# Kernel tuning notes

Hardware: AMD Instinct MI355X
Metric: run time of the kernel (lower is better)

The kernel has to match this reference:

```python
import jax, jax.numpy as jnp
import numpy as np

N = 64            # SSM state size
L = 4194304       # l_max = sequence length (2**22)
M = 4096          # chunk length for kernel construction
NCHUNK = L // M   # 1024 chunks


def setup_inputs() -> dict:
    key = jax.random.key(0)
    k0, k1, k2, k3, k4 = jax.random.split(key, 5)
    u = jax.random.normal(k0, (L, 1), jnp.float32)
    # lecun_normal: std = 1/sqrt(fan_in)
    W = jax.random.normal(k1, (N, N), jnp.float32) * np.float32(1.0 / np.sqrt(N))
    # spectral shift so bilinear-discretized Ab is stable over L steps
    A = W - 1.5 * jnp.eye(N, dtype=jnp.float32)
    B = jax.random.normal(k2, (N, 1), jnp.float32)  # fan_in = 1 -> std 1
    C = jax.random.normal(k3, (1, N), jnp.float32) * np.float32(1.0 / np.sqrt(N))
    D = jnp.ones((1,), jnp.float32)
    lo, hi = np.float32(np.log(1e-3)), np.float32(np.log(1e-1))
    log_step = jax.random.uniform(k4, (1,), jnp.float32, lo, hi)
    return {"u": u, "A": A, "B": B, "C": C, "D": D, "log_step": log_step}


def _ssm_forward(u, A, B, C, D, log_step):
    step = jnp.exp(log_step)[0]
    I = jnp.eye(N, dtype=A.dtype)
    # bilinear (Tustin) discretization
    BL = jnp.linalg.inv(I - A * (step / 2.0))
    Ab = BL @ (I + A * (step / 2.0))          # [N, N]
    Bb = (BL * step) @ B                      # [N, 1]
    Cb = C                                    # [1, N]

    # K[k] = Cb @ Ab^k @ Bb, k = 0..L-1, built in chunks of M:
    # X0[:, k] = Ab^k @ Bb for k < M
    def step_x(x, _):
        return Ab @ x, x
    _, xs = jax.lax.scan(step_x, Bb[:, 0], None, length=M)   # [M, N]
    X0 = xs.T                                                # [N, M]

    AbM = jnp.linalg.matrix_power(Ab, M)                     # Ab^M
    def step_p(P, _):
        return AbM @ P, Cb[0] @ P                            # row: Cb @ Ab^(j*M)
    _, cps = jax.lax.scan(step_p, I, None, length=NCHUNK)    # [NCHUNK, N]
    K = (cps @ X0).reshape(L, 1)                             # [L, 1]

    # FFT causal convolution (pad to 2L, pointwise multiply, crop)
    fft_size = 2 * L
    u_d = jnp.fft.rfft(jnp.pad(u, ((0, L), (0, 0))), n=fft_size, axis=0)
    K_d = jnp.fft.rfft(jnp.pad(K, ((0, L), (0, 0))), n=fft_size, axis=0)
    y = jnp.fft.irfft(u_d * K_d, n=fft_size, axis=0)[:L]
    return y + D * u


def reference(u, A, B, C, D, log_step):
    return _ssm_forward(u, A, B, C, D, log_step)
```

## Files before the change

kernel.cpp:

```cpp
#include <hip/hip_runtime.h>
#include <cmath>


#define NST 64
#define LSEQ 4194304
#define MC 256
#define NCHUNK (LSEQ / MC)
#define SEG 128
#define NSEG (NCHUNK / SEG)
#define NPOW 16

#define POW_OFF 0
#define BB_OFF (NPOW * 4096)
#define XCOL_OFF (BB_OFF + 64)
#define KL_OFF (XCOL_OFF + MC * 64)
#define RT_OFF (KL_OFF + MC)
#define F_OFF (RT_OFF + 64 * MC)
#define CARRY_OFF (F_OFF + NCHUNK * 64)
#define SEGINIT_OFF (CARRY_OFF + NSEG * 64)
#define WS_FLOATS (SEGINIT_OFF + NSEG * 64)

__device__ __forceinline__ float bcast(float x, int k) {
  return __int_as_float(__builtin_amdgcn_readlane(__float_as_int(x), k));
}

__global__ __launch_bounds__(1024) void k_setup(
    const float* __restrict__ A, const float* __restrict__ Bv,
    const float* __restrict__ Cv, const float* __restrict__ lstep,
    float* __restrict__ ws) {
  __shared__ __align__(16) float sm[8704];
  const int t = threadIdx.x;
  const float h = 0.5f * expf(lstep[0]);

  for (int idx = t; idx < 64 * 128; idx += 1024) {
    int r = idx >> 7, c = idx & 127;
    float v;
    if (c < 64)
      v = (r == c ? 1.0f : 0.0f) - h * A[r * 64 + c];
    else
      v = (r == (c - 64)) ? 1.0f : 0.0f;
    sm[r * 129 + c] = v;
  }
  __syncthreads();
  for (int k = 0; k < 64; ++k) {
    if (t < 64) sm[8256 + t] = sm[t * 129 + k];
    __syncthreads();
    float pinv = 1.0f / sm[8256 + k];
    if (t < 128) sm[k * 129 + t] *= pinv;
    __syncthreads();
    for (int idx = t; idx < 64 * 128; idx += 1024) {
      int r = idx >> 7, c = idx & 127;
      if (r != k) sm[r * 129 + c] -= sm[8256 + r] * sm[k * 129 + c];
    }
    __syncthreads();
  }

  for (int idx = t; idx < 4096; idx += 1024) {
    int r = idx >> 6, c = idx & 63;
    float acc = 0.f;
    for (int k = 0; k < 64; ++k) acc += sm[r * 129 + 64 + k] * A[k * 64 + c];
    ws[POW_OFF + r * 64 + c] = sm[r * 129 + 64 + c] + h * acc;
  }
  if (t < 64) {
    float acc = 0.f;
    for (int k = 0; k < 64; ++k) acc += sm[t * 129 + 64 + k] * Bv[k];
    ws[BB_OFF + t] = 2.0f * h * acc;
  }
  __syncthreads();

  for (int idx = t; idx < 4096; idx += 1024)
    sm[(idx >> 6) * 68 + (idx & 63)] = ws[POW_OFF + idx];
  __syncthreads();
  for (int s = 1; s < NPOW; ++s) {
    float* src = sm + ((s & 1) ? 0 : 4352);
    float* dst = sm + ((s & 1) ? 4352 : 0);
    const int r = t >> 4, c0 = (t & 15) << 2;
    float4 acc = {0.f, 0.f, 0.f, 0.f};
#pragma unroll 8
    for (int k = 0; k < 64; ++k) {
      float a = src[r * 68 + k];
      const float4 b = *(const float4*)&src[k * 68 + c0];
      acc.x += a * b.x; acc.y += a * b.y; acc.z += a * b.z; acc.w += a * b.w;
    }
    *(float4*)&dst[r * 68 + c0] = acc;
    *(float4*)&ws[POW_OFF + s * 4096 + r * 64 + c0] = acc;
    __syncthreads();
  }

  if (t < 64) {
    ws[XCOL_OFF + t] = ws[BB_OFF + t];
  } else if (t < 128) {
    int n = t - 64;
    float acc = 0.f;
    for (int k = 0; k < 64; ++k) acc += Cv[k] * ws[POW_OFF + k * 64 + n];
    ws[RT_OFF + n * MC + 0] = acc;
  }
  for (int s = 0; s < 8; ++s) {
    __syncthreads();
    for (int idx = t; idx < 4096; idx += 1024)
      sm[(idx >> 6) * 65 + (idx & 63)] = ws[POW_OFF + s * 4096 + idx];
    __syncthreads();
    const int cnt = 1 << s;
    for (int idx = t; idx < cnt * 64; idx += 1024) {
      int ir = cnt + (idx >> 6), n = idx & 63, isrc = ir - cnt;
      float xv = 0.f, rv = 0.f;
#pragma unroll 8
      for (int k = 0; k < 64; ++k) {
        xv += sm[n * 65 + k] * ws[XCOL_OFF + isrc * 64 + k];
        rv += sm[k * 65 + n] * ws[RT_OFF + k * MC + isrc];
      }
      ws[XCOL_OFF + ir * 64 + n] = xv;
      ws[RT_OFF + n * MC + ir] = rv;
    }
  }
  __syncthreads();

  {
    const int w = t >> 6, lane = t & 63;
    for (int i = w; i < MC; i += 16) {
      float p = Cv[lane] * ws[XCOL_OFF + i * 64 + lane];
#pragma unroll
      for (int m = 32; m >= 1; m >>= 1) p += __shfl_xor(p, m, 64);
      if (lane == 0) ws[KL_OFF + i] = p;
    }
  }
}

__global__ __launch_bounds__(256) void k_f(const float* __restrict__ u,
                                           float* __restrict__ ws) {
  __shared__ __align__(16) float us[16 * MC];
  const int t = threadIdx.x;
  const int c0 = blockIdx.x * 16;
  for (int idx = t; idx < 16 * MC; idx += 256)
    us[idx] = u[(size_t)c0 * MC + idx];
  __syncthreads();
  const int n = t & 63, g = t >> 6;
  const float* xc = ws + XCOL_OFF;
  const float* ug = us + g * 4 * MC;
  float a0 = 0.f, a1 = 0.f, a2 = 0.f, a3 = 0.f;
  for (int j = 0; j < MC; j += 4) {
    float x0 = xc[(MC - 1 - j) * 64 + n];
    float x1 = xc[(MC - 2 - j) * 64 + n];
    float x2 = xc[(MC - 3 - j) * 64 + n];
    float x3 = xc[(MC - 4 - j) * 64 + n];
    {
      const float4 uv = *(const float4*)&ug[0 * MC + j];
      a0 += x0 * uv.x + x1 * uv.y + x2 * uv.z + x3 * uv.w;
    }
    {
      const float4 uv = *(const float4*)&ug[1 * MC + j];
      a1 += x0 * uv.x + x1 * uv.y + x2 * uv.z + x3 * uv.w;
    }
    {
      const float4 uv = *(const float4*)&ug[2 * MC + j];
      a2 += x0 * uv.x + x1 * uv.y + x2 * uv.z + x3 * uv.w;
    }
    {
      const float4 uv = *(const float4*)&ug[3 * MC + j];
      a3 += x0 * uv.x + x1 * uv.y + x2 * uv.z + x3 * uv.w;
    }
  }
  float* Fb = ws + F_OFF + (size_t)(c0 + g * 4) * 64;
  Fb[0 * 64 + n] = a0;
  Fb[1 * 64 + n] = a1;
  Fb[2 * 64 + n] = a2;
  Fb[3 * 64 + n] = a3;
}

#define MATVEC_STEP(preg, xv, a0, a1, a2, a3)          \
  _Pragma("unroll") for (int k = 0; k < 64; k += 4) {  \
    a0 = fmaf(preg[k + 0], bcast(xv, k + 0), a0);      \
    a1 = fmaf(preg[k + 1], bcast(xv, k + 1), a1);      \
    a2 = fmaf(preg[k + 2], bcast(xv, k + 2), a2);      \
    a3 = fmaf(preg[k + 3], bcast(xv, k + 3), a3);      \
  }

__global__ __launch_bounds__(64) void k_scan1(float* __restrict__ ws) {
  __shared__ float Pl[64 * 65];
  const int n = threadIdx.x;
  for (int idx = n; idx < 4096; idx += 64)
    Pl[(idx >> 6) * 65 + (idx & 63)] = ws[POW_OFF + 8 * 4096 + idx];
  __syncthreads();
  float p[64];
#pragma unroll
  for (int k = 0; k < 64; ++k) p[k] = Pl[n * 65 + k];
  float x = 0.f;
  const float* Fp = ws + F_OFF + (size_t)blockIdx.x * SEG * 64;
  float fv = Fp[n];
  for (int c = 0; c < SEG; ++c) {
    float fnext = Fp[(c < SEG - 1 ? c + 1 : c) * 64 + n];
    float a0 = 0.f, a1 = 0.f, a2 = 0.f, a3 = 0.f;
    MATVEC_STEP(p, x, a0, a1, a2, a3)
    x = ((a0 + a1) + (a2 + a3)) + fv;
    fv = fnext;
  }
  ws[CARRY_OFF + blockIdx.x * 64 + n] = x;
}

__global__ __launch_bounds__(64) void k_scantop(float* __restrict__ ws) {
  __shared__ float Ql[64 * 65];
  const int n = threadIdx.x;
  for (int idx = n; idx < 4096; idx += 64)
    Ql[(idx >> 6) * 65 + (idx & 63)] = ws[POW_OFF + 15 * 4096 + idx];
  __syncthreads();
  float q[64];
#pragma unroll
  for (int k = 0; k < 64; ++k) q[k] = Ql[n * 65 + k];
  float x = 0.f;
  float cv = ws[CARRY_OFF + n];
  for (int s = 0; s < NSEG; ++s) {
    float cnext = ws[CARRY_OFF + (s < NSEG - 1 ? s + 1 : s) * 64 + n];
    ws[SEGINIT_OFF + s * 64 + n] = x;
    float a0 = 0.f, a1 = 0.f, a2 = 0.f, a3 = 0.f;
    MATVEC_STEP(q, x, a0, a1, a2, a3)
    x = ((a0 + a1) + (a2 + a3)) + cv;
    cv = cnext;
  }
}

__global__ __launch_bounds__(64) void k_scan2(float* __restrict__ ws) {
  __shared__ float Pl[64 * 65];
  const int n = threadIdx.x;
  for (int idx = n; idx < 4096; idx += 64)
    Pl[(idx >> 6) * 65 + (idx & 63)] = ws[POW_OFF + 8 * 4096 + idx];
  __syncthreads();
  float p[64];
#pragma unroll
  for (int k = 0; k < 64; ++k) p[k] = Pl[n * 65 + k];
  float x = ws[SEGINIT_OFF + blockIdx.x * 64 + n];
  float* Fp = ws + F_OFF + (size_t)blockIdx.x * SEG * 64;
  float fv = Fp[n];
  for (int c = 0; c < SEG; ++c) {
    float fnext = Fp[(c < SEG - 1 ? c + 1 : c) * 64 + n];
    Fp[c * 64 + n] = x;
    float a0 = 0.f, a1 = 0.f, a2 = 0.f, a3 = 0.f;
    MATVEC_STEP(p, x, a0, a1, a2, a3)
    x = ((a0 + a1) + (a2 + a3)) + fv;
    fv = fnext;
  }
}

__global__ __launch_bounds__(256) void k_final(const float* __restrict__ u,
                                               const float* __restrict__ Dv,
                                               const float* __restrict__ ws,
                                               float* __restrict__ out) {
  __shared__ __align__(16) float us[8 * MC];
  __shared__ __align__(16) float kl[MC];
  __shared__ __align__(16) float xin[8 * 64];
  const int t = threadIdx.x;
  const int c0 = blockIdx.x * 8;
  for (int idx = t; idx < 8 * MC; idx += 256)
    us[idx] = u[(size_t)c0 * MC + idx];
  kl[t] = ws[KL_OFF + t];
  for (int idx = t; idx < 8 * 64; idx += 256)
    xin[idx] = ws[F_OFF + (size_t)c0 * 64 + idx];
  __syncthreads();

  float acc[8];
#pragma unroll
  for (int cc = 0; cc < 8; ++cc) acc[cc] = 0.f;

  const float* rt = ws + RT_OFF;
#pragma unroll 4
  for (int nn = 0; nn < 64; nn += 4) {
    float r0 = rt[(nn + 0) * MC + t];
    float r1 = rt[(nn + 1) * MC + t];
    float r2 = rt[(nn + 2) * MC + t];
    float r3 = rt[(nn + 3) * MC + t];
#pragma unroll
    for (int cc = 0; cc < 8; ++cc) {
      const float4 xv = *(const float4*)&xin[cc * 64 + nn];
      acc[cc] += r0 * xv.x + r1 * xv.y + r2 * xv.z + r3 * xv.w;
    }
  }

  const int i = t;
  int j = 0;
  for (; j + 3 <= i; j += 4) {
    float k0 = kl[i - j], k1 = kl[i - j - 1], k2 = kl[i - j - 2],
          k3 = kl[i - j - 3];
#pragma unroll
    for (int cc = 0; cc < 8; ++cc) {
      const float4 uv = *(const float4*)&us[cc * MC + j];
      acc[cc] += k0 * uv.x + k1 * uv.y + k2 * uv.z + k3 * uv.w;
    }
  }
  for (; j <= i; ++j) {
    float kv = kl[i - j];
#pragma unroll
    for (int cc = 0; cc < 8; ++cc) acc[cc] += kv * us[cc * MC + j];
  }

  const float D0 = Dv[0];
#pragma unroll
  for (int cc = 0; cc < 8; ++cc)
    out[(size_t)(c0 + cc) * MC + i] = acc[cc] + D0 * us[cc * MC + i];
}

extern "C" void kernel_launch(void* const* d_in, const int* in_sizes, int n_in,
                              void* d_out, int out_size, void* d_ws,
                              size_t ws_size, hipStream_t stream) {
  (void)in_sizes; (void)n_in; (void)out_size; (void)ws_size;
  const float* u = (const float*)d_in[0];
  const float* A = (const float*)d_in[1];
  const float* B = (const float*)d_in[2];
  const float* C = (const float*)d_in[3];
  const float* D = (const float*)d_in[4];
  const float* ls = (const float*)d_in[5];
  float* ws = (float*)d_ws;
  float* out = (float*)d_out;

  hipLaunchKernelGGL(k_setup, dim3(1), dim3(1024), 0, stream, A, B, C, ls, ws);
  hipLaunchKernelGGL(k_f, dim3(NCHUNK / 16), dim3(256), 0, stream, u, ws);
  hipLaunchKernelGGL(k_scan1, dim3(NSEG), dim3(64), 0, stream, ws);
  hipLaunchKernelGGL(k_scantop, dim3(1), dim3(64), 0, stream, ws);
  hipLaunchKernelGGL(k_scan2, dim3(NSEG), dim3(64), 0, stream, ws);
  hipLaunchKernelGGL(k_final, dim3(NCHUNK / 8), dim3(256), 0, stream, u, D, ws,
                     out);
}
```

Before: 444.1 us.

## Restructure setup kernel: fused Gauss-Jordan solve, register-tiled powers, parallel Krylov generation

Rewrites the single-block setup kernel. Gauss-Jordan now reduces [I-hA | I+hA | 2hB] together, so Ab and Bb fall out directly without separate matmuls, and the elimination updates use float4 over only the remaining columns. Matrix squaring uses an 8x4 register tile over row and transposed copies, and stores only the powers that are needed (4, 8, 15). The X and R Krylov columns are built by 16 waves in parallel from seeds spaced Ab^16 apart, using register-resident matvecs, instead of log-doubling through global memory. It trims a serial, latency-bound setup phase at the cost of more shared memory and more code complexity.

```diff
diff --git a/kernel.cpp b/kernel.cpp
--- a/kernel.cpp
+++ b/kernel.cpp
@@ -8,14 +8,19 @@
 #define NCHUNK (LSEQ / MC)
 #define SEG 128
 #define NSEG (NCHUNK / SEG)
-#define NPOW 16
-
-#define POW_OFF 0
-#define BB_OFF (NPOW * 4096)
-#define XCOL_OFF (BB_OFF + 64)
-#define KL_OFF (XCOL_OFF + MC * 64)
-#define RT_OFF (KL_OFF + MC)
-#define F_OFF (RT_OFF + 64 * MC)
+
+#define ABR_OFF 0
+#define ABT_OFF 4096
+#define P4R_OFF 8192
+#define P4T_OFF 12288
+#define P8_OFF 16384
+#define P15_OFF 20480
+#define BB_OFF 24576
+#define KL_OFF 24640
+#define XCOL_OFF 24896
+#define RTT_OFF 41280
+#define RT_OFF 57664
+#define F_OFF 74048
 #define CARRY_OFF (F_OFF + NCHUNK * 64)
 #define SEGINIT_OFF (CARRY_OFF + NSEG * 64)
 #define WS_FLOATS (SEGINIT_OFF + NSEG * 64)
@@ -23,102 +28,227 @@
 __device__ __forceinline__ float bcast(float x, int k) {
   return __int_as_float(__builtin_amdgcn_readlane(__float_as_int(x), k));
 }
+
+__device__ __forceinline__ float matvec64(const float4 (&m)[16], float x) {
+  float a0 = 0.f, a1 = 0.f, a2 = 0.f, a3 = 0.f;
+#pragma unroll
+  for (int kq = 0; kq < 16; ++kq) {
+    a0 = fmaf(m[kq].x, bcast(x, 4 * kq + 0), a0);
+    a1 = fmaf(m[kq].y, bcast(x, 4 * kq + 1), a1);
+    a2 = fmaf(m[kq].z, bcast(x, 4 * kq + 2), a2);
+    a3 = fmaf(m[kq].w, bcast(x, 4 * kq + 3), a3);
+  }
+  return ((a0 + a1) + (a2 + a3));
+}
+
+__device__ __forceinline__ void load_rows(float4 (&m)[16], const float* src,
+                                          int lane) {
+#pragma unroll
+  for (int kq = 0; kq < 16; ++kq)
+    m[kq] = *(const float4*)(src + (size_t)lane * 64 + kq * 4);
+}
+
+#define CGET(v, cj) ((cj) == 0 ? (v).x : (cj) == 1 ? (v).y : (cj) == 2 ? (v).z : (v).w)
 
 __global__ __launch_bounds__(1024) void k_setup(
     const float* __restrict__ A, const float* __restrict__ Bv,
     const float* __restrict__ Cv, const float* __restrict__ lstep,
     float* __restrict__ ws) {
-  __shared__ __align__(16) float sm[8704];
+  __shared__ __align__(16) float sm[14592];
+  float* colbuf = sm + 12352;
+  float* xs = sm + 12416;
+  float* rs = sm + 13504;
   const int t = threadIdx.x;
+  const int w = t >> 6, lane = t & 63;
   const float h = 0.5f * expf(lstep[0]);
 
-  for (int idx = t; idx < 64 * 128; idx += 1024) {
-    int r = idx >> 7, c = idx & 127;
-    float v;
-    if (c < 64)
-      v = (r == c ? 1.0f : 0.0f) - h * A[r * 64 + c];
-    else
-      v = (r == (c - 64)) ? 1.0f : 0.0f;
-    sm[r * 129 + c] = v;
-  }
-  __syncthreads();
-  for (int k = 0; k < 64; ++k) {
-    if (t < 64) sm[8256 + t] = sm[t * 129 + k];
-    __syncthreads();
-    float pinv = 1.0f / sm[8256 + k];
-    if (t < 128) sm[k * 129 + t] *= pinv;
-    __syncthreads();
-    for (int idx = t; idx < 64 * 128; idx += 1024) {
-      int r = idx >> 7, c = idx & 127;
-      if (r != k) sm[r * 129 + c] -= sm[8256 + r] * sm[k * 129 + c];
-    }
-    __syncthreads();
-  }
-
+  {
+    const int r = t >> 4;
+    for (int c = t & 15; c < 144; c += 16) {
+      float v = 0.f;
+      if (c < 64)
+        v = (r == c ? 1.0f : 0.0f) - h * A[r * 64 + c];
+      else if (c < 128)
+        v = (r == (c - 64) ? 1.0f : 0.0f) + h * A[r * 64 + (c - 64)];
+      else if (c == 128)
+        v = 2.0f * h * Bv[r];
+      sm[r * 144 + c] = v;
+    }
+  }
+  __syncthreads();
+  {
+    float4* G4 = (float4*)sm;
+    for (int k = 0; k < 64; ++k) {
+      if (t < 64) colbuf[t] = sm[t * 144 + k];
+      __syncthreads();
+      const float pinv = 1.0f / colbuf[k];
+      const int r = lane;
+      const float mr = colbuf[r] * pinv;
+      for (int q = (k >> 2) + w; q <= 32; q += 16) {
+        float4 pr = G4[k * 36 + q];
+        float4 g = G4[r * 36 + q];
+        if (r == k) {
+          g.x = pr.x * pinv; g.y = pr.y * pinv;
+          g.z = pr.z * pinv; g.w = pr.w * pinv;
+        } else {
+          g.x = fmaf(-mr, pr.x, g.x); g.y = fmaf(-mr, pr.y, g.y);
+          g.z = fmaf(-mr, pr.z, g.z); g.w = fmaf(-mr, pr.w, g.w);
+        }
+        G4[r * 36 + q] = g;
+      }
+      __syncthreads();
+    }
+  }
   for (int idx = t; idx < 4096; idx += 1024) {
     int r = idx >> 6, c = idx & 63;
-    float acc = 0.f;
-    for (int k = 0; k < 64; ++k) acc += sm[r * 129 + 64 + k] * A[k * 64 + c];
-    ws[POW_OFF + r * 64 + c] = sm[r * 129 + 64 + c] + h * acc;
-  }
-  if (t < 64) {
-    float acc = 0.f;
-    for (int k = 0; k < 64; ++k) acc += sm[t * 129 + 64 + k] * Bv[k];
-    ws[BB_OFF + t] = 2.0f * h * acc;
-  }
-  __syncthreads();
-
-  for (int idx = t; idx < 4096; idx += 1024)
-    sm[(idx >> 6) * 68 + (idx & 63)] = ws[POW_OFF + idx];
-  __syncthreads();
-  for (int s = 1; s < NPOW; ++s) {
-    float* src = sm + ((s & 1) ? 0 : 4352);
-    float* dst = sm + ((s & 1) ? 4352 : 0);
-    const int r = t >> 4, c0 = (t & 15) << 2;
-    float4 acc = {0.f, 0.f, 0.f, 0.f};
+    ws[ABR_OFF + idx] = sm[r * 144 + 64 + c];
+  }
+  if (t < 64) ws[BB_OFF + t] = sm[t * 144 + 128];
+  __syncthreads();
+
+  {
+    float* AR = sm;
+    float* AT = sm + 4096;
+    float* tr = sm + 8192;
+    for (int idx = t; idx < 4096; idx += 1024) {
+      float v = ws[ABR_OFF + idx];
+      AR[idx] = v;
+      tr[(idx & 63) * 65 + (idx >> 6)] = v;
+    }
+    __syncthreads();
+    for (int idx = t; idx < 4096; idx += 1024) {
+      float v = tr[(idx >> 6) * 65 + (idx & 63)];
+      AT[idx] = v;
+      ws[ABT_OFF + idx] = v;
+    }
+  }
+  __syncthreads();
+
+  {
+    float4* AR4 = (float4*)sm;
+    float4* AT4 = (float4*)(sm + 4096);
+    const bool active = t < 128;
+    const int r0 = (t >> 4) << 3;
+    const int c0q = t & 15;
+    for (int s = 1; s <= 15; ++s) {
+      float4 acc[8];
+#pragma unroll
+      for (int j = 0; j < 8; ++j) acc[j] = {0.f, 0.f, 0.f, 0.f};
+      if (active) {
 #pragma unroll 8
-    for (int k = 0; k < 64; ++k) {
-      float a = src[r * 68 + k];
-      const float4 b = *(const float4*)&src[k * 68 + c0];
-      acc.x += a * b.x; acc.y += a * b.y; acc.z += a * b.z; acc.w += a * b.w;
-    }
-    *(float4*)&dst[r * 68 + c0] = acc;
-    *(float4*)&ws[POW_OFF + s * 4096 + r * 64 + c0] = acc;
-    __syncthreads();
-  }
-
-  if (t < 64) {
-    ws[XCOL_OFF + t] = ws[BB_OFF + t];
-  } else if (t < 128) {
-    int n = t - 64;
-    float acc = 0.f;
-    for (int k = 0; k < 64; ++k) acc += Cv[k] * ws[POW_OFF + k * 64 + n];
-    ws[RT_OFF + n * MC + 0] = acc;
-  }
-  for (int s = 0; s < 8; ++s) {
-    __syncthreads();
-    for (int idx = t; idx < 4096; idx += 1024)
-      sm[(idx >> 6) * 65 + (idx & 63)] = ws[POW_OFF + s * 4096 + idx];
-    __syncthreads();
-    const int cnt = 1 << s;
-    for (int idx = t; idx < cnt * 64; idx += 1024) {
-      int ir = cnt + (idx >> 6), n = idx & 63, isrc = ir - cnt;
-      float xv = 0.f, rv = 0.f;
-#pragma unroll 8
-      for (int k = 0; k < 64; ++k) {
-        xv += sm[n * 65 + k] * ws[XCOL_OFF + isrc * 64 + k];
-        rv += sm[k * 65 + n] * ws[RT_OFF + k * MC + isrc];
+        for (int k = 0; k < 64; ++k) {
+          const float4 b = AR4[k * 16 + c0q];
+          const float4 a0 = AT4[k * 16 + (r0 >> 2)];
+          const float4 a1 = AT4[k * 16 + (r0 >> 2) + 1];
+          acc[0].x = fmaf(a0.x, b.x, acc[0].x); acc[0].y = fmaf(a0.x, b.y, acc[0].y);
+          acc[0].z = fmaf(a0.x, b.z, acc[0].z); acc[0].w = fmaf(a0.x, b.w, acc[0].w);
+          acc[1].x = fmaf(a0.y, b.x, acc[1].x); acc[1].y = fmaf(a0.y, b.y, acc[1].y);
+          acc[1].z = fmaf(a0.y, b.z, acc[1].z); acc[1].w = fmaf(a0.y, b.w, acc[1].w);
+          acc[2].x = fmaf(a0.z, b.x, acc[2].x); acc[2].y = fmaf(a0.z, b.y, acc[2].y);
+          acc[2].z = fmaf(a0.z, b.z, acc[2].z); acc[2].w = fmaf(a0.z, b.w, acc[2].w);
+          acc[3].x = fmaf(a0.w, b.x, acc[3].x); acc[3].y = fmaf(a0.w, b.y, acc[3].y);
+          acc[3].z = fmaf(a0.w, b.z, acc[3].z); acc[3].w = fmaf(a0.w, b.w, acc[3].w);
+          acc[4].x = fmaf(a1.x, b.x, acc[4].x); acc[4].y = fmaf(a1.x, b.y, acc[4].y);
+          acc[4].z = fmaf(a1.x, b.z, acc[4].z); acc[4].w = fmaf(a1.x, b.w, acc[4].w);
+          acc[5].x = fmaf(a1.y, b.x, acc[5].x); acc[5].y = fmaf(a1.y, b.y, acc[5].y);
+          acc[5].z = fmaf(a1.y, b.z, acc[5].z); acc[5].w = fmaf(a1.y, b.w, acc[5].w);
+          acc[6].x = fmaf(a1.z, b.x, acc[6].x); acc[6].y = fmaf(a1.z, b.y, acc[6].y);
+          acc[6].z = fmaf(a1.z, b.z, acc[6].z); acc[6].w = fmaf(a1.z, b.w, acc[6].w);
+          acc[7].x = fmaf(a1.w, b.x, acc[7].x); acc[7].y = fmaf(a1.w, b.y, acc[7].y);
+          acc[7].z = fmaf(a1.w, b.z, acc[7].z); acc[7].w = fmaf(a1.w, b.w, acc[7].w);
+        }
       }
-      ws[XCOL_OFF + ir * 64 + n] = xv;
-      ws[RT_OFF + n * MC + ir] = rv;
-    }
-  }
-  __syncthreads();
-
-  {
-    const int w = t >> 6, lane = t & 63;
+      __syncthreads();
+      if (active) {
+#pragma unroll
+        for (int j = 0; j < 8; ++j) AR4[(r0 + j) * 16 + c0q] = acc[j];
+#pragma unroll
+        for (int cj = 0; cj < 4; ++cj) {
+          float4 lo = {CGET(acc[0], cj), CGET(acc[1], cj), CGET(acc[2], cj),
+                       CGET(acc[3], cj)};
+          float4 hi = {CGET(acc[4], cj), CGET(acc[5], cj), CGET(acc[6], cj),
+                       CGET(acc[7], cj)};
+          AT4[(c0q * 4 + cj) * 16 + (r0 >> 2)] = lo;
+          AT4[(c0q * 4 + cj) * 16 + (r0 >> 2) + 1] = hi;
+          if (s == 4) {
+            *(float4*)&ws[P4T_OFF + (c0q * 4 + cj) * 64 + r0] = lo;
+            *(float4*)&ws[P4T_OFF + (c0q * 4 + cj) * 64 + r0 + 4] = hi;
+          }
+        }
+        if (s == 4 || s == 8 || s == 15) {
+          const int off = (s == 4) ? P4R_OFF : (s == 8) ? P8_OFF : P15_OFF;
+#pragma unroll
+          for (int j = 0; j < 8; ++j)
+            *(float4*)&ws[off + (r0 + j) * 64 + c0q * 4] = acc[j];
+        }
+      }
+      __syncthreads();
+    }
+  }
+
+  if (w == 0 || w == 8) {
+    float4 m[16];
+    float x;
+    float* sb = (w == 0) ? xs : rs;
+    if (w == 0) {
+      load_rows(m, ws + P4R_OFF, lane);
+      x = ws[BB_OFF + lane];
+    } else {
+      load_rows(m, ws + ABT_OFF, lane);
+      x = matvec64(m, Cv[lane]);
+      load_rows(m, ws + P4T_OFF, lane);
+    }
+    sb[0 * 68 + lane] = x;
+#pragma unroll 1
+    for (int g = 1; g < 16; ++g) {
+      x = matvec64(m, x);
+      sb[g * 68 + lane] = x;
+    }
+  }
+  __syncthreads();
+
+  {
+    float4 m[16];
+    load_rows(m, ws + ABR_OFF, lane);
+    float x = xs[w * 68 + lane];
+#pragma unroll 1
+    for (int j = 0; j < 16; ++j) {
+      ws[XCOL_OFF + (size_t)(16 * w + j) * 64 + lane] = x;
+      if (j < 15) x = matvec64(m, x);
+    }
+  }
+  {
+    float4 m[16];
+    load_rows(m, ws + ABT_OFF, lane);
+    float r = rs[w * 68 + lane];
+#pragma unroll 1
+    for (int j = 0; j < 16; ++j) {
+      ws[RTT_OFF + (size_t)(16 * w + j) * 64 + lane] = r;
+      if (j < 15) r = matvec64(m, r);
+    }
+  }
+  __syncthreads();
+
+  {
+    float* tr = sm + 8192;
+    for (int blk = 0; blk < 4; ++blk) {
+      for (int idx = t; idx < 4096; idx += 1024) {
+        int il = idx >> 6, n = idx & 63;
+        tr[n * 65 + il] = ws[RTT_OFF + (size_t)(blk * 64 + il) * 64 + n];
+      }
+      __syncthreads();
+      for (int idx = t; idx < 4096; idx += 1024) {
+        int n = idx >> 6, il = idx & 63;
+        ws[RT_OFF + (size_t)n * MC + blk * 64 + il] = tr[n * 65 + il];
+      }
+      __syncthreads();
+    }
+  }
+
+  {
+    const float cv = Cv[lane];
     for (int i = w; i < MC; i += 16) {
-      float p = Cv[lane] * ws[XCOL_OFF + i * 64 + lane];
+      float p = cv * ws[XCOL_OFF + (size_t)i * 64 + lane];
 #pragma unroll
       for (int m = 32; m >= 1; m >>= 1) p += __shfl_xor(p, m, 64);
       if (lane == 0) ws[KL_OFF + i] = p;
@@ -179,7 +309,7 @@
   __shared__ float Pl[64 * 65];
   const int n = threadIdx.x;
   for (int idx = n; idx < 4096; idx += 64)
-    Pl[(idx >> 6) * 65 + (idx & 63)] = ws[POW_OFF + 8 * 4096 + idx];
+    Pl[(idx >> 6) * 65 + (idx & 63)] = ws[P8_OFF + idx];
   __syncthreads();
   float p[64];
 #pragma unroll
@@ -201,7 +331,7 @@
   __shared__ float Ql[64 * 65];
   const int n = threadIdx.x;
   for (int idx = n; idx < 4096; idx += 64)
-    Ql[(idx >> 6) * 65 + (idx & 63)] = ws[POW_OFF + 15 * 4096 + idx];
+    Ql[(idx >> 6) * 65 + (idx & 63)] = ws[P15_OFF + idx];
   __syncthreads();
   float q[64];
 #pragma unroll
@@ -222,7 +352,7 @@
   __shared__ float Pl[64 * 65];
   const int n = threadIdx.x;
   for (int idx = n; idx < 4096; idx += 64)
-    Pl[(idx >> 6) * 65 + (idx & 63)] = ws[POW_OFF + 8 * 4096 + idx];
+    Pl[(idx >> 6) * 65 + (idx & 63)] = ws[P8_OFF + idx];
   __syncthreads();
   float p[64];
 #pragma unroll
```

Result: faster. 428.2 us (-3.6%).
